# Kernel tuning notes

Measured on AMD Instinct MI355X. Metric: run time of the kernel, lower is better.

The kernel has to match this reference:

```python
import jax, jax.numpy as jnp
import numpy as np

DIM = 768
HEADS = 12
TOPK = 32


def setup_inputs() -> dict:
    key = jax.random.key(0)
    k1, k2, k3 = jax.random.split(key, 3)
    B, hw, T = 8, 576, 4
    N = hw + T * hw
    x = jax.random.normal(k1, (B, N, DIM), dtype=jnp.float32)
    qkv_w = jax.random.normal(k2, (3 * DIM, DIM), dtype=jnp.float32) * 0.02
    proj_w = jax.random.normal(k3, (DIM, DIM), dtype=jnp.float32) * 0.02
    proj_b = jnp.zeros((DIM,), dtype=jnp.float32)
    return {"x": x, "qkv_w": qkv_w, "proj_w": proj_w, "proj_b": proj_b, "T": T, "hw": hw}


def _query_topk_every_frame(attn, hw, T):
    # attn: [B, H, hw, hw + T*hw]
    B, H, n1, _ = attn.shape
    qa = attn[..., :hw]                       # [B,H,hw,hw] query self part
    ma = attn[..., hw:].reshape(B, H, n1, T, hw)  # per-frame memory scores
    vals, idx = jax.lax.top_k(ma, TOPK)       # [B,H,hw,T,K]
    cat = jnp.concatenate([qa, vals.reshape(B, H, n1, T * TOPK)], axis=-1)
    sm = jax.nn.softmax(cat, axis=-1)         # softmax over hw + T*K survivors
    qa2 = sm[..., :hw]
    tv = sm[..., hw:].reshape(B, H, n1, T, TOPK)
    # scatter normalized top-k values back into dense per-frame affinity
    bi = jnp.arange(B)[:, None, None, None, None]
    hi = jnp.arange(H)[None, :, None, None, None]
    ni = jnp.arange(n1)[None, None, :, None, None]
    ti = jnp.arange(T)[None, None, None, :, None]
    aff = jnp.zeros_like(ma).at[bi, hi, ni, ti, idx].set(tv)
    return jnp.concatenate([qa2, aff.reshape(B, H, n1, T * hw)], axis=-1)


def reference(x, qkv_w, proj_w, proj_b, T, hw):
    B, N, C = x.shape
    assert N == hw + T * hw
    hd = C // HEADS
    scale = hd ** -0.5
    qkv = (x @ qkv_w.T).reshape(B, N, 3, HEADS, hd).transpose(2, 0, 3, 1, 4)
    q, k, v = qkv[0], qkv[1], qkv[2]          # each [B,H,N,hd]
    query_q = q[:, :, :hw]                    # [B,H,hw,hd]
    attn = jnp.einsum('bhqd,bhkd->bhqk', query_q, k) * scale  # [B,H,hw,N]
    attn = _query_topk_every_frame(attn, hw, T)
    out = jnp.einsum('bhqk,bhkd->bhqd', attn, v)  # [B,H,hw,hd]
    query = out.transpose(0, 2, 1, 3).reshape(B, hw, C)
    query = query @ proj_w.T + proj_b
    # memory tokens pass through unchanged
    return jnp.concatenate([query, x[:, hw:]], axis=1)
```

## Files before the change

### kernel.cpp

```cpp
#include <hip/hip_runtime.h>
#include <hip/hip_bf16.h>


using s16x8 = __attribute__((ext_vector_type(8))) short;
using f32x4 = __attribute__((ext_vector_type(4))) float;
typedef unsigned short u16;

#define MFMA_B16(A,B,C) __builtin_amdgcn_mfma_f32_16x16x32_bf16(A,B,C,0,0,0)

__device__ __forceinline__ u16 f2bf(float f) {
  unsigned u = __float_as_uint(f);
  u += 0x7FFFu + ((u >> 16) & 1u);
  return (u16)(u >> 16);
}
__device__ __forceinline__ float bf2f(u16 h) {
  return __uint_as_float(((unsigned)h) << 16);
}
__device__ __forceinline__ int lanes_below(unsigned long long m) {
  return __builtin_amdgcn_mbcnt_hi((unsigned)(m >> 32),
         __builtin_amdgcn_mbcnt_lo((unsigned)m, 0));
}
__device__ __forceinline__ void stage16(const u16* __restrict__ g, u16* l) {
  __builtin_amdgcn_global_load_lds(
      (const __attribute__((address_space(1))) unsigned int*)g,
      (__attribute__((address_space(3))) unsigned int*)l, 16, 0, 0);
}

__global__ __launch_bounds__(256) void cvt_kernel(const float* __restrict__ src,
                                                  u16* __restrict__ dst, int n4) {
  int i = blockIdx.x * blockDim.x + threadIdx.x;
  if (i >= n4) return;
  float4 v = ((const float4*)src)[i];
  unsigned lo = (unsigned)f2bf(v.x) | ((unsigned)f2bf(v.y) << 16);
  unsigned hi = (unsigned)f2bf(v.z) | ((unsigned)f2bf(v.w) << 16);
  uint2 o; o.x = lo; o.y = hi;
  ((uint2*)dst)[i] = o;
}

__global__ __launch_bounds__(256) void copy_tail_kernel(const float* __restrict__ x,
                                                        float* __restrict__ out) {
  int i = blockIdx.x * blockDim.x + threadIdx.x;
  int b = i / 442368;
  int off = i - b * 442368;
  size_t e = (size_t)b * 552960 + 110592 + off;
  ((float4*)out)[e] = ((const float4*)x)[e];
}

template<int MODE>
__global__ __launch_bounds__(256) void gemm_nt(
    const u16* __restrict__ A, const u16* __restrict__ Bw,
    const float* __restrict__ bias,
    u16* __restrict__ qbuf, u16* __restrict__ kbuf,
    u16* __restrict__ vtb, float* __restrict__ fout)
{
  __shared__ __align__(16) u16 smem[128 * 128];
  u16* sA = smem;
  u16* sB = smem + 128 * 64;
  const int n0 = blockIdx.x * 128;
  const int m0 = blockIdx.y * 128;
  if (MODE == 0 && n0 < 768) {
    const int s = m0 % 2880;
    if (s >= 576 && s + 128 <= 2880) return;
  }
  const int tid = threadIdx.x;
  const int w = tid >> 6, lane = tid & 63;
  const int l15 = lane & 15, rg = lane >> 4;
  const int ko = rg * 8;
  const int mq = (w >> 1) * 64, nq = (w & 1) * 64;
  const int trow = tid >> 3, tcol = (tid & 7) * 8;

  f32x4 z = {0.f, 0.f, 0.f, 0.f};
  f32x4 acc[4][4];
  #pragma unroll
  for (int i = 0; i < 4; ++i)
    #pragma unroll
    for (int j = 0; j < 4; ++j) acc[i][j] = z;

  for (int k0 = 0; k0 < 768; k0 += 64) {
    __syncthreads();
    #pragma unroll
    for (int i = 0; i < 4; ++i) {
      stage16(&A[(size_t)(m0 + trow + i * 32) * 768 + k0 + tcol],
              &sA[(trow + i * 32) * 64 + tcol]);
      stage16(&Bw[(size_t)(n0 + trow + i * 32) * 768 + k0 + tcol],
              &sB[(trow + i * 32) * 64 + tcol]);
    }
    __syncthreads();
    #pragma unroll
    for (int kk = 0; kk < 2; ++kk) {
      const int ko2 = kk * 32 + ko;
      s16x8 af[4], bf[4];
      #pragma unroll
      for (int i = 0; i < 4; ++i) {
        af[i] = *(const s16x8*)&sA[(mq + i * 16 + l15) * 64 + ko2];
        bf[i] = *(const s16x8*)&sB[(nq + i * 16 + l15) * 64 + ko2];
      }
      #pragma unroll
      for (int mi = 0; mi < 4; ++mi)
        #pragma unroll
        for (int ni = 0; ni < 4; ++ni)
          acc[mi][ni] = MFMA_B16(af[mi], bf[ni], acc[mi][ni]);
    }
  }

  if (MODE == 0) {
    const int which = n0 / 768;
    const int nb = n0 % 768;
    if (which == 2) {
      __syncthreads();
      #pragma unroll
      for (int mi = 0; mi < 4; ++mi)
        #pragma unroll
        for (int ni = 0; ni < 4; ++ni)
          #pragma unroll
          for (int r = 0; r < 4; ++r)
            smem[(mq + mi * 16 + rg * 4 + r) * 128 + nq + ni * 16 + l15] =
                f2bf(acc[mi][ni][r]);
      __syncthreads();
      const int c = tid & 127, kh = tid >> 7;
      const int gm0 = m0 + kh * 64;
      const int bb = gm0 / 2880, rr0 = gm0 - bb * 2880;
      const int ng = nb + c;
      const int hh = ng >> 6, dd = ng & 63;
      u16* dst = vtb + ((size_t)((bb * 12 + hh) * 64 + dd)) * 2880 + rr0;
      #pragma unroll
      for (int seg = 0; seg < 4; ++seg) {
        u16 tmp[16];
        #pragma unroll
        for (int i = 0; i < 16; ++i)
          tmp[i] = smem[(kh * 64 + seg * 16 + i) * 128 + c];
        *(int4*)&dst[seg * 16]     = *(const int4*)&tmp[0];
        *(int4*)&dst[seg * 16 + 8] = *(const int4*)&tmp[8];
      }
    } else {
      #pragma unroll
      for (int mi = 0; mi < 4; ++mi)
        #pragma unroll
        for (int ni = 0; ni < 4; ++ni)
          #pragma unroll
          for (int r = 0; r < 4; ++r) {
            const int gm = m0 + mq + mi * 16 + rg * 4 + r;
            const int b  = gm / 2880;
            const int rr = gm - b * 2880;
            const int ng = nb + nq + ni * 16 + l15;
            const int h  = ng >> 6, d = ng & 63;
            const float cc = acc[mi][ni][r];
            if (which == 0) {
              if (rr < 576)
                qbuf[((size_t)(b * 12 + h) * 576 + rr) * 64 + d] = f2bf(cc * 0.125f);
            } else {
              kbuf[((size_t)(b * 12 + h) * 2880 + rr) * 64 + d] = f2bf(cc);
            }
          }
    }
  } else {
    #pragma unroll
    for (int mi = 0; mi < 4; ++mi)
      #pragma unroll
      for (int ni = 0; ni < 4; ++ni)
        #pragma unroll
        for (int r = 0; r < 4; ++r) {
          const int gm = m0 + mq + mi * 16 + rg * 4 + r;
          const int gn = n0 + nq + ni * 16 + l15;
          const int b = gm / 576;
          const int q = gm - b * 576;
          fout[((size_t)b * 2880 + q) * 768 + gn] = acc[mi][ni][r] + bias[gn];
        }
  }
}

__global__ __launch_bounds__(256, 6) void attn_kernel(
    const u16* __restrict__ qbuf, const u16* __restrict__ kbuf,
    const u16* __restrict__ vtb, u16* __restrict__ aout)
{
  constexpr int PST = 584;
  __shared__ __align__(16) u16 s_p[16 * PST];
  __shared__ float s_denom[16];

  const int bid = blockIdx.x;
  const int L = (bid & 7) * 432 + (bid >> 3);
  const int qt = L % 36;
  const int h  = (L / 36) % 12;
  const int b  = L / 432;
  const int bh = b * 12 + h;
  const int q0 = qt * 16;
  const int tid = threadIdx.x, w = tid >> 6, lane = tid & 63;
  const int l15 = lane & 15, rg = lane >> 4;
  const int ko = rg * 8;

  const u16* qp = qbuf + ((size_t)bh * 576 + q0) * 64;
  s16x8 aQ[2];
  aQ[0] = *(const s16x8*)&qp[l15 * 64 + ko];
  aQ[1] = *(const s16x8*)&qp[l15 * 64 + 32 + ko];

  const u16* kp = kbuf + (size_t)bh * 2880 * 64;
  const u16* vt = vtb + ((size_t)bh * 64 + w * 16 + l15) * 2880;
  f32x4 zz = {0.f, 0.f, 0.f, 0.f};
  f32x4 accO = zz;

  for (int c = 0; c < 5; ++c) {
    #pragma unroll 3
    for (int t = 0; t < 9; ++t) {
      const int wk = w * 144 + t * 16;
      const u16* kr = kp + (size_t)(c * 576 + wk + l15) * 64 + ko;
      s16x8 kf0 = *(const s16x8*)&kr[0];
      s16x8 kf1 = *(const s16x8*)&kr[32];
      f32x4 a0 = zz;
      a0 = MFMA_B16(aQ[0], kf0, a0);
      a0 = MFMA_B16(aQ[1], kf1, a0);
      #pragma unroll
      for (int r = 0; r < 4; ++r)
        s_p[(rg * 4 + r) * PST + wk + l15] =
            (u16)(__float_as_uint(__expf(a0[r])) >> 16);
    }
    __syncthreads();

    if (c == 0) {
      #pragma unroll
      for (int ri = 0; ri < 4; ++ri) {
        const int q = w * 4 + ri;
        float s = 0.f;
        #pragma unroll
        for (int j = 0; j < 9; ++j) s += bf2f(s_p[q * PST + lane + 64 * j]);
        #pragma unroll
        for (int off = 1; off < 64; off <<= 1) s += __shfl_xor(s, off);
        if (lane == 0) s_denom[q] = s;
      }
    } else {
      unsigned key[4][9];
      #pragma unroll
      for (int ri = 0; ri < 4; ++ri)
        #pragma unroll
        for (int j = 0; j < 9; ++j)
          key[ri][j] = (unsigned)s_p[(w * 4 + ri) * PST + lane + 64 * j];
      unsigned pf[4] = {0u, 0u, 0u, 0u};
      for (int bit = 14; bit >= 0; --bit) {
        int cnt[4];
        #pragma unroll
        for (int ri = 0; ri < 4; ++ri) {
          const unsigned cand = pf[ri] | (1u << bit);
          int cn = 0;
          #pragma unroll
          for (int j = 0; j < 9; ++j)
            cn += __popcll(__ballot(key[ri][j] >= cand));
          cnt[ri] = cn;
        }
        #pragma unroll
        for (int ri = 0; ri < 4; ++ri)
          if (cnt[ri] >= 32) pf[ri] |= (1u << bit);
      }
      #pragma unroll
      for (int ri = 0; ri < 4; ++ri) {
        const int q = w * 4 + ri;
        const unsigned prefix = pf[ri];
        unsigned long long eqm[9];
        int cnt_gt = 0;
        #pragma unroll
        for (int j = 0; j < 9; ++j) {
          cnt_gt += __popcll(__ballot(key[ri][j] > prefix));
          eqm[j] = __ballot(key[ri][j] == prefix);
        }
        const int rem = 32 - cnt_gt;
        int run_eq = 0;
        float dsum = 0.f;
        #pragma unroll
        for (int j = 0; j < 9; ++j) {
          const bool sel = (key[ri][j] > prefix) ||
              (key[ri][j] == prefix && run_eq + lanes_below(eqm[j]) < rem);
          const u16 raw = (u16)key[ri][j];
          dsum += sel ? bf2f(raw) : 0.f;
          s_p[q * PST + lane + 64 * j] = sel ? raw : (u16)0;
          run_eq += __popcll(eqm[j]);
        }
        #pragma unroll
        for (int off = 1; off < 64; off <<= 1) dsum += __shfl_xor(dsum, off);
        if (lane == 0) s_denom[q] += dsum;
      }
      __syncthreads();
    }

    #pragma unroll 3
    for (int k0 = 0; k0 < 576; k0 += 32) {
      s16x8 vf = *(const s16x8*)&vt[c * 576 + k0 + ko];
      s16x8 pa = *(const s16x8*)&s_p[l15 * PST + k0 + ko];
      accO = MFMA_B16(pa, vf, accO);
    }
    __syncthreads();
  }

  const int d = w * 16 + l15;
  #pragma unroll
  for (int r = 0; r < 4; ++r) {
    const int row = rg * 4 + r;
    const float val = accO[r] / s_denom[row];
    aout[((size_t)(b * 576 + q0 + row)) * 768 + h * 64 + d] = f2bf(val);
  }
}

extern "C" void kernel_launch(void* const* d_in, const int* in_sizes, int n_in,
                              void* d_out, int out_size, void* d_ws, size_t ws_size,
                              hipStream_t stream)
{
  const float* x      = (const float*)d_in[0];
  const float* qkv_w  = (const float*)d_in[1];
  const float* proj_w = (const float*)d_in[2];
  const float* proj_b = (const float*)d_in[3];
  float* out = (float*)d_out;

  char* ws = (char*)d_ws;
  size_t off = 0;
  auto alloc = [&](size_t bytes) -> void* {
    void* p = ws + off;
    off += (bytes + 255) & ~(size_t)255;
    return p;
  };
  u16* xb   = (u16*)alloc((size_t)23040 * 768 * 2);
  u16* wqb  = (u16*)alloc((size_t)2304 * 768 * 2);
  u16* wpb  = (u16*)alloc((size_t)768 * 768 * 2);
  u16* qbuf = (u16*)alloc((size_t)96 * 576 * 64 * 2);
  u16* vtb  = (u16*)alloc((size_t)96 * 64 * 2880 * 2);
  u16* aout = (u16*)alloc((size_t)4608 * 768 * 2);
  u16* kbuf = (u16*)d_out;

  cvt_kernel<<<17280, 256, 0, stream>>>(x, xb, 17694720 / 4);
  cvt_kernel<<<1728, 256, 0, stream>>>(qkv_w, wqb, 1769472 / 4);
  cvt_kernel<<<576, 256, 0, stream>>>(proj_w, wpb, 589824 / 4);
  gemm_nt<0><<<dim3(18, 180), 256, 0, stream>>>(xb, wqb, nullptr,
                                                qbuf, kbuf, vtb, nullptr);
  attn_kernel<<<3456, 256, 0, stream>>>(qbuf, kbuf, vtb, aout);
  gemm_nt<1><<<dim3(6, 36), 256, 0, stream>>>(aout, wpb, proj_b,
                                              nullptr, nullptr, nullptr, out);
  copy_tail_kernel<<<13824, 256, 0, stream>>>(x, out);
}
```

Before: 487.5 us.

## Split attention across frame chunks with partial outputs and a reduce kernel

The attention kernel now gives each of the five key chunks (query self-part plus four memory frames) its own block instead of looping over them sequentially. This gives five times more blocks, and the launch bound moves from 6 to 8 blocks per SM. Each block writes unnormalized fp32 partial outputs and partial denominators to workspace, and a new reduce kernel sums them and normalizes. The cost is an extra kernel launch, about 70MB of extra fp32 partial traffic, and a reload of the Q fragment in every block.

```diff
diff --git a/kernel.cpp b/kernel.cpp
--- a/kernel.cpp
+++ b/kernel.cpp
@@ -169,21 +169,24 @@
   }
 }
 
-__global__ __launch_bounds__(256, 6) void attn_kernel(
+__global__ __launch_bounds__(256, 8) void attn_kernel(
     const u16* __restrict__ qbuf, const u16* __restrict__ kbuf,
-    const u16* __restrict__ vtb, u16* __restrict__ aout)
+    const u16* __restrict__ vtb,
+    float* __restrict__ opart, float* __restrict__ dpart)
 {
   constexpr int PST = 584;
   __shared__ __align__(16) u16 s_p[16 * PST];
-  __shared__ float s_denom[16];
 
   const int bid = blockIdx.x;
-  const int L = (bid & 7) * 432 + (bid >> 3);
-  const int qt = L % 36;
-  const int h  = (L / 36) % 12;
-  const int b  = L / 432;
+  const int L = (bid & 7) * 2160 + (bid >> 3);
+  const int b   = L / 2160;
+  const int rem = L % 2160;
+  const int c   = rem / 432;
+  const int h   = (rem / 36) % 12;
+  const int qt  = rem % 36;
   const int bh = b * 12 + h;
   const int q0 = qt * 16;
+  const int bq = bh * 36 + qt;
   const int tid = threadIdx.x, w = tid >> 6, lane = tid & 63;
   const int l15 = lane & 15, rg = lane >> 4;
   const int ko = rg * 8;
@@ -198,102 +201,124 @@
   f32x4 zz = {0.f, 0.f, 0.f, 0.f};
   f32x4 accO = zz;
 
-  for (int c = 0; c < 5; ++c) {
-    #pragma unroll 3
-    for (int t = 0; t < 9; ++t) {
-      const int wk = w * 144 + t * 16;
-      const u16* kr = kp + (size_t)(c * 576 + wk + l15) * 64 + ko;
-      s16x8 kf0 = *(const s16x8*)&kr[0];
-      s16x8 kf1 = *(const s16x8*)&kr[32];
-      f32x4 a0 = zz;
-      a0 = MFMA_B16(aQ[0], kf0, a0);
-      a0 = MFMA_B16(aQ[1], kf1, a0);
-      #pragma unroll
-      for (int r = 0; r < 4; ++r)
-        s_p[(rg * 4 + r) * PST + wk + l15] =
-            (u16)(__float_as_uint(__expf(a0[r])) >> 16);
+  #pragma unroll 3
+  for (int t = 0; t < 9; ++t) {
+    const int wk = w * 144 + t * 16;
+    const u16* kr = kp + (size_t)(c * 576 + wk + l15) * 64 + ko;
+    s16x8 kf0 = *(const s16x8*)&kr[0];
+    s16x8 kf1 = *(const s16x8*)&kr[32];
+    f32x4 a0 = zz;
+    a0 = MFMA_B16(aQ[0], kf0, a0);
+    a0 = MFMA_B16(aQ[1], kf1, a0);
+    #pragma unroll
+    for (int r = 0; r < 4; ++r)
+      s_p[(rg * 4 + r) * PST + wk + l15] =
+          (u16)(__float_as_uint(__expf(a0[r])) >> 16);
+  }
+  __syncthreads();
+
+  if (c == 0) {
+    #pragma unroll
+    for (int ri = 0; ri < 4; ++ri) {
+      const int q = w * 4 + ri;
+      float s = 0.f;
+      #pragma unroll
+      for (int j = 0; j < 9; ++j) s += bf2f(s_p[q * PST + lane + 64 * j]);
+      #pragma unroll
+      for (int off = 1; off < 64; off <<= 1) s += __shfl_xor(s, off);
+      if (lane == 0) dpart[(size_t)(bq * 5 + c) * 16 + q] = s;
+    }
+  } else {
+    unsigned key[4][9];
+    #pragma unroll
+    for (int ri = 0; ri < 4; ++ri)
+      #pragma unroll
+      for (int j = 0; j < 9; ++j)
+        key[ri][j] = (unsigned)s_p[(w * 4 + ri) * PST + lane + 64 * j];
+    unsigned pf[4] = {0u, 0u, 0u, 0u};
+    for (int bit = 14; bit >= 0; --bit) {
+      int cnt[4];
+      #pragma unroll
+      for (int ri = 0; ri < 4; ++ri) {
+        const unsigned cand = pf[ri] | (1u << bit);
+        int cn = 0;
+        #pragma unroll
+        for (int j = 0; j < 9; ++j)
+          cn += __popcll(__ballot(key[ri][j] >= cand));
+        cnt[ri] = cn;
+      }
+      #pragma unroll
+      for (int ri = 0; ri < 4; ++ri)
+        if (cnt[ri] >= 32) pf[ri] |= (1u << bit);
+    }
+    #pragma unroll
+    for (int ri = 0; ri < 4; ++ri) {
+      const int q = w * 4 + ri;
+      const unsigned prefix = pf[ri];
+      unsigned long long eqm[9];
+      int cnt_gt = 0;
+      #pragma unroll
+      for (int j = 0; j < 9; ++j) {
+        cnt_gt += __popcll(__ballot(key[ri][j] > prefix));
+        eqm[j] = __ballot(key[ri][j] == prefix);
+      }
+      const int rem2 = 32 - cnt_gt;
+      int run_eq = 0;
+      float dsum = 0.f;
+      #pragma unroll
+      for (int j = 0; j < 9; ++j) {
+        const bool sel = (key[ri][j] > prefix) ||
+            (key[ri][j] == prefix && run_eq + lanes_below(eqm[j]) < rem2);
+        const u16 raw = (u16)key[ri][j];
+        dsum += sel ? bf2f(raw) : 0.f;
+        s_p[q * PST + lane + 64 * j] = sel ? raw : (u16)0;
+        run_eq += __popcll(eqm[j]);
+      }
+      #pragma unroll
+      for (int off = 1; off < 64; off <<= 1) dsum += __shfl_xor(dsum, off);
+      if (lane == 0) dpart[(size_t)(bq * 5 + c) * 16 + q] = dsum;
     }
     __syncthreads();
-
-    if (c == 0) {
-      #pragma unroll
-      for (int ri = 0; ri < 4; ++ri) {
-        const int q = w * 4 + ri;
-        float s = 0.f;
-        #pragma unroll
-        for (int j = 0; j < 9; ++j) s += bf2f(s_p[q * PST + lane + 64 * j]);
-        #pragma unroll
-        for (int off = 1; off < 64; off <<= 1) s += __shfl_xor(s, off);
-        if (lane == 0) s_denom[q] = s;
-      }
-    } else {
-      unsigned key[4][9];
-      #pragma unroll
-      for (int ri = 0; ri < 4; ++ri)
-        #pragma unroll
-        for (int j = 0; j < 9; ++j)
-          key[ri][j] = (unsigned)s_p[(w * 4 + ri) * PST + lane + 64 * j];
-      unsigned pf[4] = {0u, 0u, 0u, 0u};
-      for (int bit = 14; bit >= 0; --bit) {
-        int cnt[4];
-        #pragma unroll
-        for (int ri = 0; ri < 4; ++ri) {
-          const unsigned cand = pf[ri] | (1u << bit);
-          int cn = 0;
-          #pragma unroll
-          for (int j = 0; j < 9; ++j)
-            cn += __popcll(__ballot(key[ri][j] >= cand));
-          cnt[ri] = cn;
-        }
-        #pragma unroll
-        for (int ri = 0; ri < 4; ++ri)
-          if (cnt[ri] >= 32) pf[ri] |= (1u << bit);
-      }
-      #pragma unroll
-      for (int ri = 0; ri < 4; ++ri) {
-        const int q = w * 4 + ri;
-        const unsigned prefix = pf[ri];
-        unsigned long long eqm[9];
-        int cnt_gt = 0;
-        #pragma unroll
-        for (int j = 0; j < 9; ++j) {
-          cnt_gt += __popcll(__ballot(key[ri][j] > prefix));
-          eqm[j] = __ballot(key[ri][j] == prefix);
-        }
-        const int rem = 32 - cnt_gt;
-        int run_eq = 0;
-        float dsum = 0.f;
-        #pragma unroll
-        for (int j = 0; j < 9; ++j) {
-          const bool sel = (key[ri][j] > prefix) ||
-              (key[ri][j] == prefix && run_eq + lanes_below(eqm[j]) < rem);
-          const u16 raw = (u16)key[ri][j];
-          dsum += sel ? bf2f(raw) : 0.f;
-          s_p[q * PST + lane + 64 * j] = sel ? raw : (u16)0;
-          run_eq += __popcll(eqm[j]);
-        }
-        #pragma unroll
-        for (int off = 1; off < 64; off <<= 1) dsum += __shfl_xor(dsum, off);
-        if (lane == 0) s_denom[q] += dsum;
-      }
-      __syncthreads();
-    }
-
-    #pragma unroll 3
-    for (int k0 = 0; k0 < 576; k0 += 32) {
-      s16x8 vf = *(const s16x8*)&vt[c * 576 + k0 + ko];
-      s16x8 pa = *(const s16x8*)&s_p[l15 * PST + k0 + ko];
-      accO = MFMA_B16(pa, vf, accO);
-    }
-    __syncthreads();
-  }
-
+  }
+
+  #pragma unroll 3
+  for (int k0 = 0; k0 < 576; k0 += 32) {
+    s16x8 vf = *(const s16x8*)&vt[c * 576 + k0 + ko];
+    s16x8 pa = *(const s16x8*)&s_p[l15 * PST + k0 + ko];
+    accO = MFMA_B16(pa, vf, accO);
+  }
+
+  float* op = opart + (size_t)(bq * 5 + c) * 1024;
   const int d = w * 16 + l15;
   #pragma unroll
   for (int r = 0; r < 4; ++r) {
     const int row = rg * 4 + r;
-    const float val = accO[r] / s_denom[row];
-    aout[((size_t)(b * 576 + q0 + row)) * 768 + h * 64 + d] = f2bf(val);
+    op[row * 64 + d] = accO[r];
+  }
+}
+
+__global__ __launch_bounds__(256) void attn_reduce(
+    const float* __restrict__ opart, const float* __restrict__ dpart,
+    u16* __restrict__ aout)
+{
+  const int bq = blockIdx.x;
+  const int t = threadIdx.x;
+  const int b = bq / 432;
+  const int h = (bq / 36) % 12;
+  const int qt = bq % 36;
+  const float* ob = opart + (size_t)bq * 5 * 1024;
+  const float* db = dpart + (size_t)bq * 5 * 16;
+  #pragma unroll
+  for (int k2 = 0; k2 < 4; ++k2) {
+    const int e = t + k2 * 256;
+    const int row = e >> 6, d = e & 63;
+    float o = 0.f, dn = 0.f;
+    #pragma unroll
+    for (int c = 0; c < 5; ++c) {
+      o  += ob[c * 1024 + e];
+      dn += db[c * 16 + row];
+    }
+    aout[((size_t)(b * 576 + qt * 16 + row)) * 768 + h * 64 + d] = f2bf(o / dn);
   }
 }
 
@@ -314,12 +339,14 @@
     off += (bytes + 255) & ~(size_t)255;
     return p;
   };
-  u16* xb   = (u16*)alloc((size_t)23040 * 768 * 2);
-  u16* wqb  = (u16*)alloc((size_t)2304 * 768 * 2);
-  u16* wpb  = (u16*)alloc((size_t)768 * 768 * 2);
-  u16* qbuf = (u16*)alloc((size_t)96 * 576 * 64 * 2);
-  u16* vtb  = (u16*)alloc((size_t)96 * 64 * 2880 * 2);
-  u16* aout = (u16*)alloc((size_t)4608 * 768 * 2);
+  u16* xb    = (u16*)alloc((size_t)23040 * 768 * 2);
+  u16* wqb   = (u16*)alloc((size_t)2304 * 768 * 2);
+  u16* wpb   = (u16*)alloc((size_t)768 * 768 * 2);
+  u16* qbuf  = (u16*)alloc((size_t)96 * 576 * 64 * 2);
+  u16* vtb   = (u16*)alloc((size_t)96 * 64 * 2880 * 2);
+  u16* aout  = (u16*)alloc((size_t)4608 * 768 * 2);
+  float* opart = (float*)alloc((size_t)17280 * 1024 * 4);
+  float* dpart = (float*)alloc((size_t)17280 * 16 * 4);
   u16* kbuf = (u16*)d_out;
 
   cvt_kernel<<<17280, 256, 0, stream>>>(x, xb, 17694720 / 4);
@@ -327,7 +354,8 @@
   cvt_kernel<<<576, 256, 0, stream>>>(proj_w, wpb, 589824 / 4);
   gemm_nt<0><<<dim3(18, 180), 256, 0, stream>>>(xb, wqb, nullptr,
                                                 qbuf, kbuf, vtb, nullptr);
-  attn_kernel<<<3456, 256, 0, stream>>>(qbuf, kbuf, vtb, aout);
+  attn_kernel<<<17280, 256, 0, stream>>>(qbuf, kbuf, vtb, opart, dpart);
+  attn_reduce<<<3456, 256, 0, stream>>>(opart, dpart, aout);
   gemm_nt<1><<<dim3(6, 36), 256, 0, stream>>>(aout, wpb, proj_b,
                                               nullptr, nullptr, nullptr, out);
   copy_tail_kernel<<<13824, 256, 0, stream>>>(x, out);
```

Result: no change. 487.3 us (-0.1%).
